# Performance work log

Measured on AMD Instinct MI355X. Metric: run time of the kernel, lower is better.

Reference implementation:

```python
import jax, jax.numpy as jnp
import numpy as np

B, N, C, H, SR = 4, 4096, 512, 8, 2
HD = C // H           # head_dim = 64
SCALE = HD ** -0.5
EPS = 1e-5


def setup_inputs() -> dict:
    key = jax.random.key(0)
    ks = jax.random.split(key, 6)
    s = 0.02
    return {
        "x": jax.random.normal(ks[0], (B, N, C), jnp.float32),
        # weights stored [in, out] (transposed vs torch nn.Linear)
        "w_qkv": jax.random.normal(ks[1], (C, 3 * C), jnp.float32) * s,
        "w_proj": jax.random.normal(ks[2], (C, C), jnp.float32) * s,
        "b_proj": jnp.zeros((C,), jnp.float32),
        # depthwise conv: OIHW with I=1, feature_group_count=C
        "w_sr_conv": jax.random.normal(ks[3], (C, 1, SR, SR), jnp.float32) * s,
        "b_sr_conv": jnp.zeros((C,), jnp.float32),
        "sr_norm_scale": jnp.ones((C,), jnp.float32),
        "sr_norm_bias": jnp.zeros((C,), jnp.float32),
        "w_sr_linear": jax.random.normal(ks[4], (C, HD), jnp.float32) * s,
        "b_sr_linear": jnp.zeros((HD,), jnp.float32),
    }


def reference(x, w_qkv, w_proj, b_proj, w_sr_conv, b_sr_conv,
              sr_norm_scale, sr_norm_bias, w_sr_linear, b_sr_linear):
    Bx, Nx, Cx = x.shape
    # qkv projection (no bias), split into heads
    qkv = (x @ w_qkv).reshape(Bx, Nx, 3, H, HD).transpose(2, 0, 3, 1, 4)  # [3,B,H,N,HD]
    q, k, v = qkv[0], qkv[1], qkv[2]

    # spatial-reduction branch (sr_ratio > 1)
    S = int(Nx ** 0.5)
    x_ = x.transpose(0, 2, 1).reshape(Bx, Cx, S, S)
    x_ = jax.lax.conv_general_dilated(
        x_, w_sr_conv, window_strides=(SR, SR), padding='VALID',
        dimension_numbers=('NCHW', 'OIHW', 'NCHW'), feature_group_count=Cx)
    x_ = x_ + b_sr_conv[None, :, None, None]
    x_ = x_.reshape(Bx, Cx, -1).transpose(0, 2, 1)  # [B, M, C], M = (S/SR)^2
    # LayerNorm over C
    mu = jnp.mean(x_, axis=-1, keepdims=True)
    var = jnp.var(x_, axis=-1, keepdims=True)
    x_ = (x_ - mu) * jax.lax.rsqrt(var + EPS) * sr_norm_scale + sr_norm_bias
    x_ = x_ @ w_sr_linear + b_sr_linear  # [B, M, HD]

    # K/V compression: softmax-weighted pooling of k and v by x_ scores
    scores_k = jax.nn.softmax(jnp.einsum('bmd,bhnd->bhmn', x_, k), axis=-1)
    k = jnp.einsum('bhmn,bhnd->bhmd', scores_k, k)  # [B,H,M,HD]
    scores_v = jax.nn.softmax(jnp.einsum('bmd,bhnd->bhmn', x_, v), axis=-1)
    v = jnp.einsum('bhmn,bhnd->bhmd', scores_v, v)  # [B,H,M,HD]

    # standard attention against compressed K/V
    attn = jax.nn.softmax(jnp.einsum('bhnd,bhmd->bhnm', q, k) * SCALE, axis=-1)
    out = jnp.einsum('bhnm,bhmd->bhnd', attn, v)        # [B,H,N,HD]
    out = out.transpose(0, 2, 1, 3).reshape(Bx, Nx, Cx)  # [B,N,C]
    return out @ w_proj + b_proj
```

## Files before the change

### kernel.cpp

```cpp
#include <hip/hip_runtime.h>

typedef float f32x4 __attribute__((ext_vector_type(4)));
typedef short bf16x8 __attribute__((ext_vector_type(8)));
typedef _Float16 f16x8 __attribute__((ext_vector_type(8)));
typedef __fp16 fp16x2 __attribute__((ext_vector_type(2)));

constexpr int kB  = 4;
constexpr int kN  = 4096;
constexpr int kC  = 512;
constexpr int kH  = 8;
constexpr int kHD = 64;
constexpr int kM  = 1024;
constexpr int kC3 = 1536;

__device__ inline unsigned pkh(float a, float b) {
    union { fp16x2 h; unsigned u; } u;
    u.h = __builtin_amdgcn_cvt_pkrtz(a, b);
    return u.u;
}

__global__ __launch_bounds__(256) void cvt_f16(
    const float* __restrict__ X, _Float16* __restrict__ Y, int n4)
{
    int i = blockIdx.x * 256 + threadIdx.x;
    if (i >= n4) return;
    float4 v = ((const float4*)X)[i];
    union { _Float16 h[4]; short4 s; } u;
    u.h[0] = (_Float16)v.x; u.h[1] = (_Float16)v.y;
    u.h[2] = (_Float16)v.z; u.h[3] = (_Float16)v.w;
    ((short4*)Y)[i] = u.s;
}

__global__ __launch_bounds__(256) void wcvtT16(
    const float* __restrict__ W, int K, int N, _Float16* __restrict__ T16)
{
    __shared__ float T[64][65];
    const int n0 = blockIdx.x * 64, k0 = blockIdx.y * 64;
    const int t = threadIdx.x;
#pragma unroll
    for (int i = 0; i < 4; i++) {
        int c = t + i * 256;
        int row = c >> 4, col4 = (c & 15) * 4;
        *(float4*)&T[row][col4] = *(const float4*)&W[(size_t)(k0 + row) * N + n0 + col4];
    }
    __syncthreads();
#pragma unroll
    for (int i = 0; i < 4; i++) {
        int c = t + i * 256;
        int nrow = c >> 4, kc4 = (c & 15) * 4;
        union { _Float16 h[4]; short4 s; } u;
        u.h[0] = (_Float16)T[kc4 + 0][nrow];
        u.h[1] = (_Float16)T[kc4 + 1][nrow];
        u.h[2] = (_Float16)T[kc4 + 2][nrow];
        u.h[3] = (_Float16)T[kc4 + 3][nrow];
        *(short4*)&T16[(size_t)(n0 + nrow) * K + k0 + kc4] = u.s;
    }
}

__global__ __launch_bounds__(256) void transpose_hd(
    const short* __restrict__ s0, const short* __restrict__ s1,
    short* __restrict__ d0, short* __restrict__ d1, int nTok)
{
    __shared__ short T[64][72];
    const short* src = blockIdx.z == 0 ? s0 : s1;
    short*       dst = blockIdx.z == 0 ? d0 : d1;
    const int n0 = blockIdx.x * 64, bh = blockIdx.y;
    const int t = threadIdx.x;
#pragma unroll
    for (int i = 0; i < 2; i++) {
        int c = t + i * 256;
        int row = c >> 3, j = (c & 7) * 8;
        *(bf16x8*)&T[row][j] = *(const bf16x8*)&src[((size_t)bh * nTok + n0 + row) * 64 + j];
    }
    __syncthreads();
#pragma unroll
    for (int i = 0; i < 2; i++) {
        int c = t + i * 256;
        int drow = c >> 3, j = (c & 7) * 8;
        bf16x8 v;
#pragma unroll
        for (int q = 0; q < 8; q++) v[q] = T[j + q][drow];
        *(bf16x8*)&dst[((size_t)bh * 64 + drow) * nTok + n0 + j] = v;
    }
}

__global__ __launch_bounds__(256) void gemm_f16(
    const _Float16* __restrict__ A, const _Float16* __restrict__ B,
    int Md, int Nd, int Kd, int mode,
    const float* __restrict__ bias, float* __restrict__ Cf,
    _Float16* __restrict__ q, _Float16* __restrict__ k, _Float16* __restrict__ v)
{
    __shared__ _Float16 Ash[128][40], Bsh[128][40];
    const int t = threadIdx.x, lane = t & 63, L = lane & 15, quad = lane >> 4;
    const int wave = t >> 6, wm = wave >> 1, wn = wave & 1;
    const int bm = blockIdx.y * 128, bn = blockIdx.x * 128;

    f32x4 acc[4][4];
#pragma unroll
    for (int i = 0; i < 4; i++)
#pragma unroll
        for (int j = 0; j < 4; j++) acc[i][j] = (f32x4){0.f, 0.f, 0.f, 0.f};

    for (int k0 = 0; k0 < Kd; k0 += 32) {
#pragma unroll
        for (int i = 0; i < 2; i++) {
            int c = t + i * 256;
            int row = c >> 2, j = (c & 3) * 8;
            *(f16x8*)&Ash[row][j] = *(const f16x8*)&A[(size_t)(bm + row) * Kd + k0 + j];
            *(f16x8*)&Bsh[row][j] = *(const f16x8*)&B[(size_t)(bn + row) * Kd + k0 + j];
        }
        __syncthreads();
        f16x8 af[4];
#pragma unroll
        for (int mi = 0; mi < 4; mi++)
            af[mi] = *(const f16x8*)&Ash[wm * 64 + mi * 16 + L][quad * 8];
#pragma unroll
        for (int ni = 0; ni < 4; ni++) {
            f16x8 bf = *(const f16x8*)&Bsh[wn * 64 + ni * 16 + L][quad * 8];
#pragma unroll
            for (int mi = 0; mi < 4; mi++)
                acc[mi][ni] = __builtin_amdgcn_mfma_f32_16x16x32_f16(af[mi], bf, acc[mi][ni], 0, 0, 0);
        }
        __syncthreads();
    }

    if (mode == 0) {
#pragma unroll
        for (int ni = 0; ni < 4; ni++) {
            int col = bn + wn * 64 + ni * 16 + L;
            float bb = bias ? bias[col] : 0.f;
#pragma unroll
            for (int mi = 0; mi < 4; mi++)
#pragma unroll
                for (int r = 0; r < 4; r++) {
                    int row = bm + wm * 64 + mi * 16 + quad * 4 + r;
                    Cf[(size_t)row * Nd + col] = acc[mi][ni][r] + bb;
                }
        }
    } else {
#pragma unroll
        for (int ni = 0; ni < 4; ni++) {
            int col = bn + wn * 64 + ni * 16 + L;
            int s = col >> 9, h = (col >> 6) & 7, d = col & 63;
            _Float16* dst = s == 0 ? q : s == 1 ? k : v;
#pragma unroll
            for (int mi = 0; mi < 4; mi++)
#pragma unroll
                for (int r = 0; r < 4; r++) {
                    int row = bm + wm * 64 + mi * 16 + quad * 4 + r;
                    int b = row >> 12, n = row & 4095;
                    size_t idx = (((size_t)b * 8 + h) * 4096 + n) * 64 + d;
                    dst[idx] = (_Float16)acc[mi][ni][r];
                }
        }
    }
}

__global__ __launch_bounds__(256) void sr_fused(
    const float* __restrict__ x, const float* __restrict__ wconv,
    const float* __restrict__ bconv, const float* __restrict__ gamma,
    const float* __restrict__ beta, const float* __restrict__ wlin,
    const float* __restrict__ blin, _Float16* __restrict__ xsr)
{
    __shared__ float nbuf[512];
    __shared__ float red[8];
    __shared__ float stats[2];
    __shared__ float pbuf[4][64];

    const int m = blockIdx.x, b = blockIdx.y;
    const int oy = m >> 5, ox = m & 31;
    const int t = threadIdx.x;
    const float* xb = x + (size_t)b * kN * kC;

    float vals[2], s = 0.f, sq = 0.f;
#pragma unroll
    for (int i = 0; i < 2; i++) {
        int c = t + i * 256;
        float acc = bconv[c];
#pragma unroll
        for (int dy = 0; dy < 2; dy++)
#pragma unroll
            for (int dx = 0; dx < 2; dx++) {
                int n = (oy * 2 + dy) * 64 + (ox * 2 + dx);
                acc += xb[(size_t)n * kC + c] * wconv[c * 4 + dy * 2 + dx];
            }
        vals[i] = acc;
        s += acc; sq += acc * acc;
    }
#pragma unroll
    for (int off = 32; off > 0; off >>= 1) {
        s  += __shfl_down(s,  off);
        sq += __shfl_down(sq, off);
    }
    if ((t & 63) == 0) { red[t >> 6] = s; red[4 + (t >> 6)] = sq; }
    __syncthreads();
    if (t == 0) {
        float ts = red[0] + red[1] + red[2] + red[3];
        float tq = red[4] + red[5] + red[6] + red[7];
        float mean = ts * (1.f / 512.f);
        float var  = tq * (1.f / 512.f) - mean * mean;
        stats[0] = mean;
        stats[1] = rsqrtf(var + 1e-5f);
    }
    __syncthreads();
    const float mean = stats[0], rstd = stats[1];
#pragma unroll
    for (int i = 0; i < 2; i++) {
        int c = t + i * 256;
        nbuf[c] = (vals[i] - mean) * rstd * gamma[c] + beta[c];
    }
    __syncthreads();
    const int d = t & 63, part = t >> 6;
    float p = 0.f;
    for (int c = part * 128; c < (part + 1) * 128; c++)
        p += nbuf[c] * wlin[c * 64 + d];
    pbuf[part][d] = p;
    __syncthreads();
    if (t < 64) {
        float o = pbuf[0][t] + pbuf[1][t] + pbuf[2][t] + pbuf[3][t] + blin[t];
        xsr[((size_t)b * kM + m) * kHD + t] = (_Float16)o;
    }
}

__global__ __launch_bounds__(256, 4) void flash_mfma(
    const _Float16* __restrict__ Q, long q_bs, long q_hs,
    const _Float16* __restrict__ K0, const _Float16* __restrict__ K1,
    long k_bs, long k_hs,
    const _Float16* __restrict__ VT0, const _Float16* __restrict__ VT1,
    long v_bs, long v_hs, int v_rs,
    _Float16* __restrict__ O,
    long o_bs, long o_hs, long o_rs, int o_cs,
    int nKtot, int nChunks, float scale, float fixedMax, int kvMerge,
    float* __restrict__ Opart, float* __restrict__ MLpart)
{
    __shared__ _Float16 Ks[64][72];
    __shared__ _Float16 VTs[64][72];
    __shared__ _Float16 Pbuf[4][32][72];
    const int t = threadIdx.x, lane = t & 63, L = lane & 15, quad = lane >> 4;
    const int wave = t >> 6;
    const int h = blockIdx.y;
    int b, which, nB;
    if (kvMerge) { b = blockIdx.z >> 1; which = blockIdx.z & 1; nB = gridDim.z >> 1; }
    else         { b = blockIdx.z;      which = 0;              nB = gridDim.z; }
    const int nMblk = gridDim.x / nChunks;
    const int mblk = blockIdx.x / nChunks, chunk = blockIdx.x % nChunks;
    const int m0 = mblk * 128;
    const int nkc = nKtot / nChunks, nbeg = chunk * nkc, nend = nbeg + nkc;
    const float cl2 = scale * 1.44269504089f;
    const float nmc = -fixedMax * 1.44269504089f;

    const _Float16* K_ = (which ? K1 : K0) + (size_t)b * k_bs + (size_t)h * k_hs;
    const _Float16* V_ = (which ? VT1 : VT0) + (size_t)b * v_bs + (size_t)h * v_hs;

    f16x8 qf[2][2];
#pragma unroll
    for (int s = 0; s < 2; s++) {
        const size_t qrow = (size_t)b * q_bs + (size_t)h * q_hs
                          + (size_t)(m0 + wave * 32 + s * 16 + L) * 64;
        qf[s][0] = *(const f16x8*)&Q[qrow + quad * 8];
        qf[s][1] = *(const f16x8*)&Q[qrow + 32 + quad * 8];
    }

    f32x4 Oacc[2][4];
#pragma unroll
    for (int s = 0; s < 2; s++)
#pragma unroll
        for (int i = 0; i < 4; i++) Oacc[s][i] = (f32x4){0.f, 0.f, 0.f, 0.f};
    float li[2] = {0.f, 0.f};

    _Float16 (*Pw)[72] = Pbuf[wave];

    const int sr = t >> 3, sj = (t & 7) * 8;
    f16x8 kp0, kp1, vp0, vp1;
    kp0 = *(const f16x8*)&K_[(size_t)(nbeg + sr) * 64 + sj];
    kp1 = *(const f16x8*)&K_[(size_t)(nbeg + sr + 32) * 64 + sj];
    vp0 = *(const f16x8*)&V_[(size_t)sr * v_rs + nbeg + sj];
    vp1 = *(const f16x8*)&V_[(size_t)(sr + 32) * v_rs + nbeg + sj];

    for (int n0 = nbeg; n0 < nend; n0 += 64) {
        *(f16x8*)&Ks[sr][sj]       = kp0;
        *(f16x8*)&Ks[sr + 32][sj]  = kp1;
        *(f16x8*)&VTs[sr][sj]      = vp0;
        *(f16x8*)&VTs[sr + 32][sj] = vp1;
        __syncthreads();

        int nn = (n0 + 64 < nend) ? n0 + 64 : nbeg;
        kp0 = *(const f16x8*)&K_[(size_t)(nn + sr) * 64 + sj];
        kp1 = *(const f16x8*)&K_[(size_t)(nn + sr + 32) * 64 + sj];
        vp0 = *(const f16x8*)&V_[(size_t)sr * v_rs + nn + sj];
        vp1 = *(const f16x8*)&V_[(size_t)(sr + 32) * v_rs + nn + sj];

        f32x4 St[2][4];
#pragma unroll
        for (int c = 0; c < 4; c++) {
            f16x8 k0 = *(const f16x8*)&Ks[c * 16 + L][quad * 8];
            f16x8 k1 = *(const f16x8*)&Ks[c * 16 + L][32 + quad * 8];
#pragma unroll
            for (int s = 0; s < 2; s++) {
                f32x4 a = (f32x4){0.f, 0.f, 0.f, 0.f};
                a = __builtin_amdgcn_mfma_f32_16x16x32_f16(k0, qf[s][0], a, 0, 0, 0);
                a = __builtin_amdgcn_mfma_f32_16x16x32_f16(k1, qf[s][1], a, 0, 0, 0);
                St[s][c] = a;
            }
        }

        unsigned pk[2][4][2];
#pragma unroll
        for (int s = 0; s < 2; s++) {
            float sum = 0.f;
#pragma unroll
            for (int c = 0; c < 4; c++)
#pragma unroll
                for (int r = 0; r < 4; r++) {
                    float p = exp2f(fmaf(St[s][c][r], cl2, nmc));
                    St[s][c][r] = p;
                    sum += p;
                }
            li[s] += sum;
#pragma unroll
            for (int c = 0; c < 4; c++) {
                pk[s][c][0] = pkh(St[s][c][0], St[s][c][1]);
                pk[s][c][1] = pkh(St[s][c][2], St[s][c][3]);
            }
        }

#pragma unroll
        for (int s = 0; s < 2; s++)
#pragma unroll
            for (int c = 0; c < 4; c++) {
                uint2 w2;
                w2.x = pk[s][c][0];
                w2.y = pk[s][c][1];
                *(uint2*)&Pw[s * 16 + L][c * 16 + quad * 4] = w2;
            }

#pragma unroll
        for (int nch = 0; nch < 2; nch++) {
            f16x8 pt0 = *(const f16x8*)&Pw[L][nch * 32 + quad * 8];
            f16x8 pt1 = *(const f16x8*)&Pw[16 + L][nch * 32 + quad * 8];
#pragma unroll
            for (int dch = 0; dch < 4; dch++) {
                f16x8 vt = *(const f16x8*)&VTs[dch * 16 + L][nch * 32 + quad * 8];
                Oacc[0][dch] = __builtin_amdgcn_mfma_f32_16x16x32_f16(vt, pt0, Oacc[0][dch], 0, 0, 0);
                Oacc[1][dch] = __builtin_amdgcn_mfma_f32_16x16x32_f16(vt, pt1, Oacc[1][dch], 0, 0, 0);
            }
        }
        __syncthreads();
    }

    float lt[2];
#pragma unroll
    for (int s = 0; s < 2; s++) {
        float v = li[s];
        v += __shfl_xor(v, 16);
        v += __shfl_xor(v, 32);
        lt[s] = v;
    }

    if (Opart) {
        int pid = (((which * nB + b) * gridDim.y + h) * nMblk + mblk) * nChunks + chunk;
        float* Ob = Opart + (size_t)pid * (128 * 64);
        float* Mb = MLpart + (size_t)pid * 256;
#pragma unroll
        for (int s = 0; s < 2; s++) {
            int mloc = wave * 32 + s * 16 + L;
#pragma unroll
            for (int dch = 0; dch < 4; dch++)
                *(f32x4*)&Ob[mloc * 64 + dch * 16 + quad * 4] = Oacc[s][dch];
            if (quad == 0) { Mb[mloc] = fixedMax; Mb[128 + mloc] = lt[s]; }
        }
    } else {
#pragma unroll
        for (int s = 0; s < 2; s++) {
            float inv = 1.f / lt[s];
            size_t base = (size_t)b * o_bs + (size_t)h * o_hs
                        + (size_t)(m0 + wave * 32 + s * 16 + L) * o_rs;
#pragma unroll
            for (int dch = 0; dch < 4; dch++)
#pragma unroll
                for (int r = 0; r < 4; r++) {
                    int d = dch * 16 + quad * 4 + r;
                    O[base + (size_t)d * o_cs] = (_Float16)(Oacc[s][dch][r] * inv);
                }
        }
    }
}

__global__ __launch_bounds__(256) void flash_combine(
    const float* __restrict__ Opart, const float* __restrict__ MLpart,
    int nMblk, int nChunks, float cl2,
    _Float16* __restrict__ O, long o_bs, long o_hs, long o_rs, int o_cs)
{
    const int t = threadIdx.x;
    const int b = blockIdx.z, h = blockIdx.y;
    const int qm = blockIdx.x * 4 + (t >> 6), d = t & 63;
    const int mblk = qm >> 7, qloc = qm & 127;
    const int pb = ((b * gridDim.y + h) * nMblk + mblk) * nChunks;
    float mf = -INFINITY;
    for (int c = 0; c < nChunks; c++)
        mf = fmaxf(mf, MLpart[(size_t)(pb + c) * 256 + qloc]);
    float num = 0.f, den = 0.f;
    for (int c = 0; c < nChunks; c++) {
        float mc = MLpart[(size_t)(pb + c) * 256 + qloc];
        float lc = MLpart[(size_t)(pb + c) * 256 + 128 + qloc];
        float w = exp2f((mc - mf) * cl2);
        den += lc * w;
        num += Opart[(size_t)(pb + c) * 8192 + qloc * 64 + d] * w;
    }
    size_t addr = (size_t)b * o_bs + (size_t)h * o_hs + (size_t)qm * o_rs + (size_t)d * o_cs;
    O[addr] = (_Float16)(num / den);
}

extern "C" void kernel_launch(void* const* d_in, const int* in_sizes, int n_in,
                              void* d_out, int out_size, void* d_ws, size_t ws_size,
                              hipStream_t stream)
{
    const float* x      = (const float*)d_in[0];
    const float* w_qkv  = (const float*)d_in[1];
    const float* w_proj = (const float*)d_in[2];
    const float* b_proj = (const float*)d_in[3];
    const float* w_conv = (const float*)d_in[4];
    const float* b_conv = (const float*)d_in[5];
    const float* g_ln   = (const float*)d_in[6];
    const float* b_ln   = (const float*)d_in[7];
    const float* w_lin  = (const float*)d_in[8];
    const float* b_lin  = (const float*)d_in[9];
    float* out = (float*)d_out;
    (void)in_sizes; (void)n_in; (void)out_size; (void)ws_size;

    short* p = (short*)d_ws;
    size_t off = 0;
    auto alloc = [&](size_t n) { short* r = p + off; off += n; return r; };

    const size_t TN = (size_t)kB * kH * kN * kHD;
    const size_t TM = (size_t)kB * kH * kM * kHD;

    _Float16* xf16 = (_Float16*)alloc((size_t)kB * kN * kC);
    _Float16* ao   = xf16;

    _Float16* wq16 = (_Float16*)alloc((size_t)kC3 * kC);
    _Float16* wp16 = (_Float16*)alloc((size_t)kC * kC);
    _Float16* qh  = (_Float16*)alloc(TN);
    _Float16* kh  = (_Float16*)alloc(TN);
    _Float16* vh  = (_Float16*)alloc(TN);
    _Float16* kT  = (_Float16*)alloc(TN);
    _Float16* vT  = (_Float16*)alloc(TN);
    _Float16* xsr = (_Float16*)alloc((size_t)kB * kM * kHD);
    _Float16* kc  = (_Float16*)alloc(TM);
    _Float16* vcT = (_Float16*)alloc(TM);
    float* MLpart = (float*)alloc((size_t)2048 * 256 * 2);
    float* Opart  = (float*)alloc((size_t)2048 * 8192 * 2);

    const int NCH = 4;

    cvt_f16<<<(kB * kN * kC / 4 + 255) / 256, 256, 0, stream>>>(
        x, xf16, kB * kN * kC / 4);

    wcvtT16<<<dim3(kC3 / 64, kC / 64), 256, 0, stream>>>(w_qkv, kC, kC3, wq16);
    wcvtT16<<<dim3(kC / 64, kC / 64), 256, 0, stream>>>(w_proj, kC, kC, wp16);

    gemm_f16<<<dim3(kC3 / 128, kB * kN / 128), 256, 0, stream>>>(
        xf16, wq16, kB * kN, kC3, kC, 1, nullptr, nullptr, qh, kh, vh);

    transpose_hd<<<dim3(kN / 64, kB * kH, 2), 256, 0, stream>>>(
        (const short*)kh, (const short*)vh, (short*)kT, (short*)vT, kN);

    sr_fused<<<dim3(kM, kB), 256, 0, stream>>>(
        x, w_conv, b_conv, g_ln, b_ln, w_lin, b_lin, xsr);

    flash_mfma<<<dim3(8 * NCH, kH, kB * 2), 256, 0, stream>>>(
        xsr, (long)kM * kHD, 0L,
        kh, vh, (long)kH * kN * kHD, (long)kN * kHD,
        kT, vT, (long)kH * kHD * kN, (long)kHD * kN, kN,
        nullptr, 0L, 0L, 0L, 0,
        kN, NCH, 1.0f, 6.0f, 1, Opart, MLpart);
    flash_combine<<<dim3(kM / 4, kH, kB), 256, 0, stream>>>(
        Opart, MLpart, 8, NCH, 1.44269504089f,
        kc, (long)kH * kM * kHD, (long)kM * kHD, 64L, 1);
    flash_combine<<<dim3(kM / 4, kH, kB), 256, 0, stream>>>(
        Opart + (size_t)1024 * 8192, MLpart + (size_t)1024 * 256, 8, NCH,
        1.44269504089f,
        vcT, (long)kH * kHD * kM, (long)kHD * kM, 1L, kM);

    flash_mfma<<<dim3(32, kH, kB), 256, 0, stream>>>(
        qh, (long)kH * kN * kHD, (long)kN * kHD,
        kc, kc, (long)kH * kM * kHD, (long)kM * kHD,
        vcT, vcT, (long)kH * kHD * kM, (long)kHD * kM, kM,
        ao, (long)kN * kC, 64L, (long)kC, 1,
        kM, 1, 0.125f, 2.0f, 0, nullptr, nullptr);

    gemm_f16<<<dim3(kC / 128, kB * kN / 128), 256, 0, stream>>>(
        ao, wp16, kB * kN, kC, kC, 0, b_proj, out,
        nullptr, nullptr, nullptr);
}
```

Before: 436.8 us.

## Keep softmax P in registers via permlane swaps instead of LDS round-trip

Drops the per-wave LDS P buffer. The packed fp16 probabilities are reshuffled across lanes with v_permlane32_swap/v_permlane16_swap so they form the B operand of the PV MFMA directly. Row sums are now accumulated with v_dot2_f32_f16 against packed ones, and the exp and pack work is fused right after each QK MFMA. Removing the LDS also allows raising launch bounds to 5 blocks per SM, at the cost of tighter register limits and sums taken from fp16-rounded values.

```diff
diff --git a/kernel.cpp b/kernel.cpp
--- a/kernel.cpp
+++ b/kernel.cpp
@@ -17,6 +17,28 @@
     union { fp16x2 h; unsigned u; } u;
     u.h = __builtin_amdgcn_cvt_pkrtz(a, b);
     return u.u;
+}
+
+__device__ inline float fdot2a(unsigned ph, unsigned ones, float acc) {
+    asm("v_dot2_f32_f16 %0, %1, %2, %0" : "+v"(acc) : "v"(ph), "v"(ones));
+    return acc;
+}
+
+__device__ inline void swap32p(unsigned &a, unsigned &b) {
+#if __has_builtin(__builtin_amdgcn_permlane32_swap)
+    auto r = __builtin_amdgcn_permlane32_swap(a, b, false, false);
+    a = r[0]; b = r[1];
+#else
+    asm volatile("v_permlane32_swap_b32 %0, %1" : "+v"(a), "+v"(b));
+#endif
+}
+__device__ inline void swap16p(unsigned &a, unsigned &b) {
+#if __has_builtin(__builtin_amdgcn_permlane16_swap)
+    auto r = __builtin_amdgcn_permlane16_swap(a, b, false, false);
+    a = r[0]; b = r[1];
+#else
+    asm volatile("v_permlane16_swap_b32 %0, %1" : "+v"(a), "+v"(b));
+#endif
 }
 
 __global__ __launch_bounds__(256) void cvt_f16(
@@ -222,7 +244,7 @@
     }
 }
 
-__global__ __launch_bounds__(256, 4) void flash_mfma(
+__global__ __launch_bounds__(256, 5) void flash_mfma(
     const _Float16* __restrict__ Q, long q_bs, long q_hs,
     const _Float16* __restrict__ K0, const _Float16* __restrict__ K1,
     long k_bs, long k_hs,
@@ -235,7 +257,6 @@
 {
     __shared__ _Float16 Ks[64][72];
     __shared__ _Float16 VTs[64][72];
-    __shared__ _Float16 Pbuf[4][32][72];
     const int t = threadIdx.x, lane = t & 63, L = lane & 15, quad = lane >> 4;
     const int wave = t >> 6;
     const int h = blockIdx.y;
@@ -248,6 +269,7 @@
     const int nkc = nKtot / nChunks, nbeg = chunk * nkc, nend = nbeg + nkc;
     const float cl2 = scale * 1.44269504089f;
     const float nmc = -fixedMax * 1.44269504089f;
+    const unsigned kOnes = 0x3C003C00u;
 
     const _Float16* K_ = (which ? K1 : K0) + (size_t)b * k_bs + (size_t)h * k_hs;
     const _Float16* V_ = (which ? VT1 : VT0) + (size_t)b * v_bs + (size_t)h * v_hs;
@@ -267,8 +289,6 @@
 #pragma unroll
         for (int i = 0; i < 4; i++) Oacc[s][i] = (f32x4){0.f, 0.f, 0.f, 0.f};
     float li[2] = {0.f, 0.f};
-
-    _Float16 (*Pw)[72] = Pbuf[wave];
 
     const int sr = t >> 3, sj = (t & 7) * 8;
     f16x8 kp0, kp1, vp0, vp1;
@@ -290,7 +310,7 @@
         vp0 = *(const f16x8*)&V_[(size_t)sr * v_rs + nn + sj];
         vp1 = *(const f16x8*)&V_[(size_t)(sr + 32) * v_rs + nn + sj];
 
-        f32x4 St[2][4];
+        unsigned d0[2][4], d1[2][4];
 #pragma unroll
         for (int c = 0; c < 4; c++) {
             f16x8 k0 = *(const f16x8*)&Ks[c * 16 + L][quad * 8];
@@ -300,49 +320,38 @@
                 f32x4 a = (f32x4){0.f, 0.f, 0.f, 0.f};
                 a = __builtin_amdgcn_mfma_f32_16x16x32_f16(k0, qf[s][0], a, 0, 0, 0);
                 a = __builtin_amdgcn_mfma_f32_16x16x32_f16(k1, qf[s][1], a, 0, 0, 0);
-                St[s][c] = a;
+                float p0 = exp2f(fmaf(a[0], cl2, nmc));
+                float p1 = exp2f(fmaf(a[1], cl2, nmc));
+                float p2 = exp2f(fmaf(a[2], cl2, nmc));
+                float p3 = exp2f(fmaf(a[3], cl2, nmc));
+                d0[s][c] = pkh(p0, p1);
+                d1[s][c] = pkh(p2, p3);
+                li[s] = fdot2a(d0[s][c], kOnes, li[s]);
+                li[s] = fdot2a(d1[s][c], kOnes, li[s]);
             }
         }
 
-        unsigned pk[2][4][2];
-#pragma unroll
-        for (int s = 0; s < 2; s++) {
-            float sum = 0.f;
-#pragma unroll
-            for (int c = 0; c < 4; c++)
-#pragma unroll
-                for (int r = 0; r < 4; r++) {
-                    float p = exp2f(fmaf(St[s][c][r], cl2, nmc));
-                    St[s][c][r] = p;
-                    sum += p;
-                }
-            li[s] += sum;
-#pragma unroll
-            for (int c = 0; c < 4; c++) {
-                pk[s][c][0] = pkh(St[s][c][0], St[s][c][1]);
-                pk[s][c][1] = pkh(St[s][c][2], St[s][c][3]);
+        f16x8 pt[2][2];
+#pragma unroll
+        for (int s = 0; s < 2; s++)
+#pragma unroll
+            for (int h2 = 0; h2 < 2; h2++) {
+                unsigned a0 = d0[s][h2 * 2], b0 = d0[s][h2 * 2 + 1];
+                swap32p(a0, b0); swap16p(a0, b0);
+                unsigned a1 = d1[s][h2 * 2], b1 = d1[s][h2 * 2 + 1];
+                swap32p(a1, b1); swap16p(a1, b1);
+                union { unsigned u[4]; f16x8 v; } U;
+                U.u[0] = a0; U.u[1] = a1; U.u[2] = b0; U.u[3] = b1;
+                pt[s][h2] = U.v;
             }
-        }
-
-#pragma unroll
-        for (int s = 0; s < 2; s++)
-#pragma unroll
-            for (int c = 0; c < 4; c++) {
-                uint2 w2;
-                w2.x = pk[s][c][0];
-                w2.y = pk[s][c][1];
-                *(uint2*)&Pw[s * 16 + L][c * 16 + quad * 4] = w2;
-            }
-
-#pragma unroll
-        for (int nch = 0; nch < 2; nch++) {
-            f16x8 pt0 = *(const f16x8*)&Pw[L][nch * 32 + quad * 8];
-            f16x8 pt1 = *(const f16x8*)&Pw[16 + L][nch * 32 + quad * 8];
+
+#pragma unroll
+        for (int h2 = 0; h2 < 2; h2++) {
 #pragma unroll
             for (int dch = 0; dch < 4; dch++) {
-                f16x8 vt = *(const f16x8*)&VTs[dch * 16 + L][nch * 32 + quad * 8];
-                Oacc[0][dch] = __builtin_amdgcn_mfma_f32_16x16x32_f16(vt, pt0, Oacc[0][dch], 0, 0, 0);
-                Oacc[1][dch] = __builtin_amdgcn_mfma_f32_16x16x32_f16(vt, pt1, Oacc[1][dch], 0, 0, 0);
+                f16x8 vt = *(const f16x8*)&VTs[dch * 16 + L][h2 * 32 + quad * 8];
+                Oacc[0][dch] = __builtin_amdgcn_mfma_f32_16x16x32_f16(vt, pt[0][h2], Oacc[0][dch], 0, 0, 0);
+                Oacc[1][dch] = __builtin_amdgcn_mfma_f32_16x16x32_f16(vt, pt[1][h2], Oacc[1][dch], 0, 0, 0);
             }
         }
         __syncthreads();
```

New measurement: 423.0 us. 1.03x faster.
